# Performance work log

Measured on AMD Instinct MI355X. Metric: run time of the kernel, lower is better.

The kernel has to match this reference:

```python
import jax, jax.numpy as jnp
import numpy as np

LAM = 0.7      # lambda_param
GAM = 2.0      # gamma (weight upper bound)
ALPHA = 0.1    # age modulation scale
FGAM = 0.1     # fusion_gamma
SIGMAS = jnp.array([0.1, 0.5, 1.0, 2.0], dtype=jnp.float32)  # multi-kernel sigmas


def setup_inputs() -> dict:
    key = jax.random.key(0)
    ks = jax.random.split(key, 12)
    B, C, D, H, W, K = 12, 64, 32, 32, 32, 32
    mid, red = C // 2, C // 4
    Z = jax.random.normal(ks[0], (B, C, D, H, W), jnp.float32)
    masks = (jax.random.uniform(ks[1], (K, D, H, W)) > 0.5).astype(jnp.float32)
    masks = masks.at[:, 0, 0, 0].set(1.0)  # guarantee every region non-empty
    labels = jnp.arange(B, dtype=jnp.int32) % 3  # 4 samples each of CN/MCI/AD
    ages = 50.0 + 40.0 * jax.random.uniform(ks[2], (B,), jnp.float32)
    prior_weights = 1.0 + 0.1 * jax.random.normal(ks[3], (K,), jnp.float32)
    struct_w = 0.05 * jax.random.normal(ks[4], (mid, C), jnp.float32)
    noise_w = 0.05 * jax.random.normal(ks[5], (mid, C), jnp.float32)
    up_w = 0.05 * jax.random.normal(ks[6], (C, mid), jnp.float32)
    region_w = 0.05 * jax.random.normal(ks[7], (C, C, 3, 3, 3), jnp.float32)
    m_w1 = 0.05 * jax.random.normal(ks[8], (red, C), jnp.float32)
    m_b1 = jnp.zeros((red,), jnp.float32)
    m_w2 = 0.05 * jax.random.normal(ks[9], (C, red), jnp.float32)
    m_b2 = jnp.zeros((C,), jnp.float32)
    return dict(Z=Z, masks=masks, labels=labels, ages=ages, prior_weights=prior_weights,
                struct_w=struct_w, noise_w=noise_w, up_w=up_w, region_w=region_w,
                m_w1=m_w1, m_b1=m_b1, m_w2=m_w2, m_b2=m_b2)


def _mmd_pair(kern, ca, cb):
    # kern: [S,K,B,B] RBF kernels; ca/cb: [B] float class indicators.
    # Unbiased MMD^2 per region, averaged over sigmas -> [K].
    m = ca.sum()
    n = cb.sum()
    Kaa = jnp.einsum('skij,i,j->sk', kern, ca, ca)
    da = jnp.einsum('skii,i->sk', kern, ca)
    Kbb = jnp.einsum('skij,i,j->sk', kern, cb, cb)
    db = jnp.einsum('skii,i->sk', kern, cb)
    t1 = (Kaa - da) / (m * (m - 1.0))
    t2 = (Kbb - db) / (n * (n - 1.0))
    t3 = jnp.einsum('skij,i,j->sk', kern, ca, cb) * (-2.0 / (m * n))
    return (t1 + t2 + t3).mean(0)


def _forward(Z, masks, labels, ages, prior_weights, struct_w, noise_w, up_w,
             region_w, m_w1, m_b1, m_w2, m_b2):
    B, C = Z.shape[:2]
    K = masks.shape[0]
    # --- region-specific aggregation (fused segment-reduce over masks) ---
    msum = masks.sum((1, 2, 3))                                   # [K]
    rf = jnp.einsum('bcdhw,kdhw->bkc', Z, masks) / (msum[None, :, None] + 1e-6)
    # --- multi-class multi-kernel MMD per region ---
    x2 = jnp.sum(rf * rf, -1)                                     # [B,K]
    ip = jnp.einsum('ikc,jkc->kij', rf, rf)                       # [K,B,B]
    d2 = jnp.maximum(x2.T[:, :, None] + x2.T[:, None, :] - 2.0 * ip, 0.0)
    kern = jnp.exp(-d2[None] / (2.0 * SIGMAS[:, None, None, None] ** 2))  # [S,K,B,B]
    c_cn = (labels == 0).astype(jnp.float32)
    c_mci = (labels == 1).astype(jnp.float32)
    c_ad = (labels == 2).astype(jnp.float32)
    D_mmd = (_mmd_pair(kern, c_ad, c_cn) + _mmd_pair(kern, c_mci, c_cn)
             + _mmd_pair(kern, c_ad, c_mci))                      # [K]
    max_mmd = jnp.maximum(D_mmd.max(), 1e-6)
    nm = jnp.clip(D_mmd / max_mmd, 0.0)
    # symmetric KL between prior and MMD-evidence distributions (batchmean -> /K)
    lp = jax.nn.log_softmax(prior_weights)
    lq = jax.nn.log_softmax(nm)
    p = jnp.exp(lp)
    q = jnp.exp(lq)
    reg = 0.5 * jnp.sum(q * (lq - lp)) / K + 0.5 * jnp.sum(p * (lp - lq)) / K
    # --- prior-guided adaptive spatial weights ---
    base = LAM * prior_weights + (1.0 - LAM) * nm
    af = 1.0 + jax.nn.softplus(ALPHA * (ages - 50.0))             # [B]
    Wk = jax.nn.softmax(jnp.clip(base[None, :] * af[:, None], 0.0, GAM), axis=1)
    spatial = jnp.einsum('bk,kdhw->bdhw', Wk, masks)[:, None]     # [B,1,D,H,W]
    # --- orthogonal decomposition ---
    cs = jnp.einsum('oc,bcdhw->bodhw', struct_w, Z)               # 1x1x1 conv
    cnoise = jnp.einsum('oc,bcdhw->bodhw', noise_w, Z)
    s = cs.reshape(B, cs.shape[1], -1)
    n = cnoise.reshape(B, cnoise.shape[1], -1)
    eps = 1e-8
    cos = jnp.sum(s * n, -1) / (jnp.maximum(jnp.linalg.norm(s, axis=-1), eps)
                                * jnp.maximum(jnp.linalg.norm(n, axis=-1), eps))
    ortho = jnp.abs(cos).mean()
    Z_clean = jnp.einsum('oc,bcdhw->bodhw', up_w, cs)
    # --- region base field + 3x3x3 conv + channel modulation ---
    Zrb = jnp.einsum('bkc,kdhw->bcdhw', rf, masks)
    Zrec = jax.lax.conv_general_dilated(
        Zrb, region_w, (1, 1, 1), 'SAME',
        dimension_numbers=('NCDHW', 'OIDHW', 'NCDHW'))
    h = jax.nn.relu(jnp.einsum('bkc,rc->bkr', rf, m_w1) + m_b1)
    mod = jax.nn.softplus(jnp.einsum('bkr,cr->bkc', h, m_w2) + m_b2)  # [B,K,C]
    Zmod = Zrec * jnp.einsum('bkc,kdhw->bcdhw', mod, masks)
    Z_out = Z_clean + FGAM * (Zmod * spatial)
    return rf, spatial, Z_out, reg + ortho


def reference(Z, masks, labels, ages, prior_weights, struct_w, noise_w, up_w,
              region_w, m_w1, m_b1, m_w2, m_b2):
    return _forward(Z, masks, labels, ages, prior_weights, struct_w, noise_w,
                    up_w, region_w, m_w1, m_b1, m_w2, m_b2)
```

## Files before the change

kernel.cpp:

```cpp
#include <hip/hip_runtime.h>
#include <hip/hip_bf16.h>
#include <math.h>

#define REG_OFF    0
#define ORTHO_OFF  1
#define FLAG_OFF   2
#define MSUM_OFF   4
#define RF_OFF     64
#define G_OFF      24640
#define WKW_OFF    73792
#define MODTB_OFF  74176
#define M1TTH_OFF  86464
#define M1TTL_OFF  88512
#define WKCB_OFF   90560
#define IPK_OFF    422336
#define WS_TOTAL   426944
#define ZERO_FLOATS 73792

#define RF_OUT   0
#define SPAT_OUT 24576
#define ZOUT_OUT 417792
#define SCAL_OUT 25583616

typedef unsigned short u16;
typedef short bh8 __attribute__((ext_vector_type(8)));
typedef float fv4 __attribute__((ext_vector_type(4)));

__device__ __forceinline__ float bf2f(u16 u) {
  union { unsigned int i; float f; } x; x.i = ((unsigned int)u) << 16; return x.f;
}
__device__ __forceinline__ u16 f2bf(float f) {
  unsigned int u = __float_as_uint(f);
  return (u16)((u + 0x7fffu + ((u >> 16) & 1u)) >> 16);
}
__device__ __forceinline__ float ldin(const void* p, size_t i, bool f32) {
  return f32 ? ((const float*)p)[i] : bf2f(((const u16*)p)[i]);
}
__device__ __forceinline__ bh8 bits2bf8(unsigned int mbits) {
  union { bh8 v; unsigned int w[4]; } u;
#pragma unroll
  for (int j = 0; j < 4; j++) {
    unsigned int tt = mbits >> (2 * j);
    u.w[j] = ((tt & 1u) | ((tt & 2u) << 15)) * 0x3F80u;
  }
  return u.v;
}

__global__ void k_probe(const void* __restrict__ Z, float* __restrict__ ws) {
  int t = threadIdx.x;
  const u16* s = (const u16*)Z;
  float mx = 0.f;
  for (int i = t; i < 8192; i += 256) {
    float a = fabsf(bf2f(s[i]));
    if (!(a < 1e30f)) a = 3e38f;
    mx = fmaxf(mx, a);
  }
  __shared__ float r[256];
  r[t] = mx; __syncthreads();
  for (int o = 128; o > 0; o >>= 1) { if (t < o) r[t] = fmaxf(r[t], r[t + o]); __syncthreads(); }
  if (t == 0) ws[FLAG_OFF] = (r[0] > 1e6f) ? 1.f : 0.f;
}

__global__ void k_msum(const void* __restrict__ masks, float* __restrict__ ws) {
  int k = blockIdx.x, t = threadIdx.x;
  bool f32 = ws[FLAG_OFF] > 0.5f;
  float s = 0.f;
  for (int v = t; v < 32768; v += 256) s += ldin(masks, ((size_t)k << 15) + v, f32);
  __shared__ float red[256];
  red[t] = s; __syncthreads();
  for (int off = 128; off > 0; off >>= 1) { if (t < off) red[t] += red[t + off]; __syncthreads(); }
  if (t == 0) ws[MSUM_OFF + k] = red[0];
}

__global__ __launch_bounds__(256) void k_rfgram(const void* __restrict__ Z,
                                                const void* __restrict__ masks,
                                                float* __restrict__ ws) {
  __shared__ float Zt[64][68];
  __shared__ float Mt[64][36];
  int b = blockIdx.y, t = threadIdx.x;
  bool f32 = ws[FLAG_OFF] > 0.5f;
  int ci = t & 15, gj = t >> 4;
  int c0 = ci << 2, c20 = gj << 2, k0 = gj << 1;
  float accG[16], accR[8];
#pragma unroll
  for (int i = 0; i < 16; i++) accG[i] = 0.f;
#pragma unroll
  for (int i = 0; i < 8; i++) accR[i] = 0.f;
  int vs = blockIdx.x << 9;
  for (int t8 = 0; t8 < 8; t8++) {
    int vb = vs + (t8 << 6);
    __syncthreads();
    if (f32) {
      const float* Zf = (const float*)Z;
      const float* Mf = (const float*)masks;
#pragma unroll
      for (int i = 0; i < 8; i++) {
        int idx = (i << 8) + t, c = idx >> 5, v2 = (idx & 31) << 1;
        float2 u = *(const float2*)(Zf + (((size_t)(b << 6) + c) << 15) + vb + v2);
        Zt[v2][c] = u.x; Zt[v2 + 1][c] = u.y;
      }
#pragma unroll
      for (int i = 0; i < 4; i++) {
        int idx = (i << 8) + t, k = idx >> 5, v2 = (idx & 31) << 1;
        float2 u = *(const float2*)(Mf + ((size_t)k << 15) + vb + v2);
        Mt[v2][k] = u.x; Mt[v2 + 1][k] = u.y;
      }
    } else {
      const u16* Zs = (const u16*)Z;
      const u16* Ms = (const u16*)masks;
#pragma unroll
      for (int i = 0; i < 8; i++) {
        int idx = (i << 8) + t, c = idx >> 5, v2 = (idx & 31) << 1;
        unsigned int u = *(const unsigned int*)(Zs + (((size_t)(b << 6) + c) << 15) + vb + v2);
        Zt[v2][c]     = bf2f((u16)(u & 0xffff));
        Zt[v2 + 1][c] = bf2f((u16)(u >> 16));
      }
#pragma unroll
      for (int i = 0; i < 4; i++) {
        int idx = (i << 8) + t, k = idx >> 5, v2 = (idx & 31) << 1;
        unsigned int u = *(const unsigned int*)(Ms + ((size_t)k << 15) + vb + v2);
        Mt[v2][k]     = bf2f((u16)(u & 0xffff));
        Mt[v2 + 1][k] = bf2f((u16)(u >> 16));
      }
    }
    __syncthreads();
    for (int vt = 0; vt < 64; vt++) {
      float4 z1 = *(const float4*)&Zt[vt][c0];
      float4 z2 = *(const float4*)&Zt[vt][c20];
      float2 m2 = *(const float2*)&Mt[vt][k0];
      float z1a[4] = {z1.x, z1.y, z1.z, z1.w};
      float z2a[4] = {z2.x, z2.y, z2.z, z2.w};
      float m2a[2] = {m2.x, m2.y};
#pragma unroll
      for (int i = 0; i < 4; i++) {
#pragma unroll
        for (int j = 0; j < 4; j++) accG[(i << 2) + j] += z1a[i] * z2a[j];
#pragma unroll
        for (int kk = 0; kk < 2; kk++) accR[(i << 1) + kk] += z1a[i] * m2a[kk];
      }
    }
  }
  float* Gd = ws + G_OFF + (b << 12);
  float* Rd = ws + RF_OFF + (b << 11);
#pragma unroll
  for (int i = 0; i < 4; i++) {
#pragma unroll
    for (int j = 0; j < 4; j++) atomicAdd(Gd + ((c0 + i) << 6) + c20 + j, accG[(i << 2) + j]);
#pragma unroll
    for (int kk = 0; kk < 2; kk++) atomicAdd(Rd + ((k0 + kk) << 6) + c0 + i, accR[(i << 1) + kk]);
  }
}

__global__ void k_scale_rf(float* __restrict__ ws, float* __restrict__ out) {
  int i = blockIdx.x * 256 + threadIdx.x;
  int k = (i >> 6) & 31;
  float v = ws[RF_OFF + i] / (ws[MSUM_OFF + k] + 1e-6f);
  ws[RF_OFF + i] = v;
  out[RF_OUT + i] = v;
}

__global__ void k_ipk(float* __restrict__ ws) {
  __shared__ float rfk[12][65];
  int k = blockIdx.x, t = threadIdx.x;
  for (int i = t; i < 768; i += 256) {
    int b = i >> 6, c = i & 63;
    rfk[b][c] = ws[RF_OFF + (((size_t)(b << 5) + k) << 6) + c];
  }
  __syncthreads();
  if (t < 144) {
    int i = t / 12, j = t - (t / 12) * 12;
    float s = 0.f;
#pragma unroll
    for (int c = 0; c < 64; c++) s += rfk[i][c] * rfk[j][c];
    ws[IPK_OFF + k * 144 + t] = s;
  }
}

__global__ void k_mmdw(const int* __restrict__ labels, const void* __restrict__ ages,
                       const void* __restrict__ prior, float* __restrict__ ws) {
  __shared__ float IPL[32 * 145];
  __shared__ float dpart[128];
  __shared__ float Dm[32], nms[32], bases[32], pwl[32];
  __shared__ int labs[12];
  int t = threadIdx.x;
  bool f32 = ws[FLAG_OFF] > 0.5f;
  if (t < 12) labs[t] = labels[t];
  for (int i = t; i < 4608; i += 256) {
    int k = i / 144, r = i - k * 144;
    IPL[k * 145 + r] = ws[IPK_OFF + i];
  }
  __syncthreads();
  if (t < 128) {
    int k = t >> 2, s = t & 3;
    const float inv2s2[4] = {50.f, 2.f, 0.5f, 0.125f};
    float inv = inv2s2[s];
    const float* pk = IPL + k * 145;
    float c0 = 0.f, c1 = 0.f, c2 = 0.f;
#pragma unroll
    for (int i = 0; i < 12; i++) {
      int li = labs[i];
      c0 += (li == 0) ? 1.f : 0.f;
      c1 += (li == 1) ? 1.f : 0.f;
      c2 += (li == 2) ? 1.f : 0.f;
    }
    float s00=0,s01=0,s02=0,s10=0,s11=0,s12=0,s20=0,s21=0,s22=0;
    float dg0=0, dg1=0, dg2=0;
    for (int i = 0; i < 12; i++) {
      int li = labs[i];
      float x2i = pk[i * 13];
      float r0=0, r1=0, r2=0, dge=0;
      for (int j = 0; j < 12; j++) {
        float d2 = fmaxf(x2i + pk[j * 13] - 2.f * pk[i * 12 + j], 0.f);
        float e = expf(-d2 * inv);
        int lj = labs[j];
        r0 += (lj == 0) ? e : 0.f;
        r1 += (lj == 1) ? e : 0.f;
        r2 += (lj == 2) ? e : 0.f;
        if (j == i) dge = e;
      }
      if (li == 0)      { s00 += r0; s01 += r1; s02 += r2; dg0 += dge; }
      else if (li == 1) { s10 += r0; s11 += r1; s12 += r2; dg1 += dge; }
      else              { s20 += r0; s21 += r1; s22 += r2; dg2 += dge; }
    }
    float ta = (s22 - dg2) / (c2 * (c2 - 1.f));
    float tb = (s00 - dg0) / (c0 * (c0 - 1.f));
    float tc = (s11 - dg1) / (c1 * (c1 - 1.f));
    float dsum = (ta + tb - 2.f * s20 / (c2 * c0))
               + (tc + tb - 2.f * s10 / (c1 * c0))
               + (ta + tc - 2.f * s21 / (c2 * c1));
    dpart[t] = dsum;
  }
  __syncthreads();
  if (t < 32) {
    Dm[t] = (dpart[t * 4] + dpart[t * 4 + 1] + dpart[t * 4 + 2] + dpart[t * 4 + 3]) * 0.25f;
    pwl[t] = (float)ldin(prior, t, f32);
  }
  __syncthreads();
  if (t == 0) {
    float mx = 1e-6f;
    for (int k = 0; k < 32; k++) mx = fmaxf(mx, Dm[k]);
    float nmax = -1e30f, pmax = -1e30f;
    for (int k = 0; k < 32; k++) {
      nms[k] = fmaxf(Dm[k] / mx, 0.f);
      nmax = fmaxf(nmax, nms[k]);
      pmax = fmaxf(pmax, pwl[k]);
    }
    float nse = 0.f, pse = 0.f;
    for (int k = 0; k < 32; k++) { nse += expf(nms[k] - nmax); pse += expf(pwl[k] - pmax); }
    float lns = logf(nse), lps = logf(pse);
    float reg = 0.f;
    for (int k = 0; k < 32; k++) {
      float lqk = nms[k] - nmax - lns;
      float lpk = pwl[k] - pmax - lps;
      reg += 0.5f * (expf(lqk) * (lqk - lpk) + expf(lpk) * (lpk - lqk));
    }
    ws[REG_OFF] = reg / 32.f;
    for (int k = 0; k < 32; k++) bases[k] = 0.7f * pwl[k] + 0.3f * nms[k];
  }
  __syncthreads();
  if (t < 12) {
    float x = 0.1f * (ldin(ages, t, f32) - 50.f);
    float af = 1.f + fmaxf(x, 0.f) + log1pf(expf(-fabsf(x)));
    float w[32];
    float mx = -1e30f;
#pragma unroll
    for (int k = 0; k < 32; k++) {
      float v = fminf(fmaxf(bases[k] * af, 0.f), 2.f);
      w[k] = v; mx = fmaxf(mx, v);
    }
    float se = 0.f;
#pragma unroll
    for (int k = 0; k < 32; k++) se += expf(w[k] - mx);
#pragma unroll
    for (int k = 0; k < 32; k++) ws[WKW_OFF + (t << 5) + k] = expf(w[k] - mx) / se;
  }
}

__global__ __launch_bounds__(64) void k_mod(const void* __restrict__ m_w1, const void* __restrict__ m_b1,
                                            const void* __restrict__ m_w2, const void* __restrict__ m_b2,
                                            float* __restrict__ ws) {
  __shared__ float W1[16][65];
  __shared__ float W2T[16][64];
  __shared__ float B1[16], B2[64], RL[64], H[16];
  int bk = blockIdx.x, t = threadIdx.x;
  int bb = bk >> 5, kk = bk & 31;
  bool f32 = ws[FLAG_OFF] > 0.5f;
  for (int i = t; i < 1024; i += 64) {
    W1[i >> 6][i & 63] = ldin(m_w1, i, f32);
    W2T[i & 15][i >> 4] = ldin(m_w2, i, f32);
  }
  if (t < 16) B1[t] = ldin(m_b1, t, f32);
  B2[t] = ldin(m_b2, t, f32);
  RL[t] = ws[RF_OFF + (bk << 6) + t];
  __syncthreads();
  if (t < 16) {
    float s = B1[t];
#pragma unroll
    for (int c = 0; c < 64; c++) s += RL[c] * W1[t][c];
    H[t] = fmaxf(s, 0.f);
  }
  __syncthreads();
  {
    int c = t;
    float s = B2[c];
#pragma unroll
    for (int rr = 0; rr < 16; rr++) s += H[rr] * W2T[rr][c];
    float mv = fmaxf(s, 0.f) + log1pf(expf(-fabsf(s)));
    ((u16*)(ws + MODTB_OFF))[((size_t)bb * 64 + c) * 32 + kk] = f2bf(mv);
  }
}

__global__ void k_m1t(const void* __restrict__ struct_w, const void* __restrict__ up_w,
                      float* __restrict__ ws) {
  __shared__ float UPT[32][64];
  __shared__ float ST[32][64];
  int t = threadIdx.x, blk = blockIdx.x;
  bool f32 = ws[FLAG_OFF] > 0.5f;
  for (int i = t; i < 2048; i += 256) {
    UPT[i & 31][i >> 5] = ldin(up_w, i, f32);
    ST[i >> 6][i & 63] = ldin(struct_w, i, f32);
  }
  __syncthreads();
  int idx = (blk << 8) + t;
  int cin = idx >> 6, co = idx & 63;
  float s = 0.f;
#pragma unroll
  for (int j = 0; j < 32; j++) s += UPT[j][co] * ST[j][cin];
  u16 hi = f2bf(s);
  ((u16*)(ws + M1TTH_OFF))[co * 64 + cin] = hi;
  ((u16*)(ws + M1TTL_OFF))[co * 64 + cin] = f2bf(s - bf2f(hi));
}

__global__ void k_ortho(const void* __restrict__ sw, const void* __restrict__ nw,
                        float* __restrict__ ws) {
  int b = blockIdx.x >> 5, o = blockIdx.x & 31, c = threadIdx.x;
  bool f32 = ws[FLAG_OFF] > 0.5f;
  const float* Gb = ws + G_OFF + (b << 12);
  float ts = 0.f, tn = 0.f;
  for (int c2 = 0; c2 < 64; c2++) {
    float g = Gb[(c << 6) + c2];
    ts += g * ldin(sw, (o << 6) + c2, f32);
    tn += g * ldin(nw, (o << 6) + c2, f32);
  }
  float swc = ldin(sw, (o << 6) + c, f32);
  float nwc = ldin(nw, (o << 6) + c, f32);
  float ds = swc * tn, ss = swc * ts, nn = nwc * tn;
  for (int off = 32; off > 0; off >>= 1) {
    ds += __shfl_down(ds, off);
    ss += __shfl_down(ss, off);
    nn += __shfl_down(nn, off);
  }
  if (c == 0) {
    ss = fmaxf(ss, 0.f); nn = fmaxf(nn, 0.f);
    float cosv = ds / (fmaxf(sqrtf(ss), 1e-8f) * fmaxf(sqrtf(nn), 1e-8f));
    atomicAdd(ws + ORTHO_OFF, fabsf(cosv) * (1.f / 384.f));
  }
}

__global__ void k_wk(const void* __restrict__ rw, float* __restrict__ ws) {
  int bk = blockIdx.x;
  int b = bk >> 5, k = bk & 31;
  int t = threadIdx.x;
  bool f32 = ws[FLAG_OFF] > 0.5f;
  __shared__ float rl[64];
  if (t < 64) rl[t] = ws[RF_OFF + (bk << 6) + t];
  __syncthreads();
  u16* dst = (u16*)(ws + WKCB_OFF);
  for (int idx = t; idx < 1728; idx += 256) {
    int o = idx / 27, d = idx - o * 27;
    float s = 0.f;
    for (int c = 0; c < 64; c++) s += rl[c] * ldin(rw, (size_t)o * 1728 + c * 27 + d, f32);
    dst[(((size_t)b * 64 + o) * 27 + d) * 32 + k] = f2bf(s);
  }
}

__global__ void k_spatial(const void* __restrict__ masks, const float* __restrict__ ws,
                          float* __restrict__ out) {
  int b = blockIdx.y, t = threadIdx.x;
  bool f32 = ws[FLAG_OFF] > 0.5f;
  __shared__ float wl[32];
  if (t < 32) wl[t] = ws[WKW_OFF + (b << 5) + t];
  __syncthreads();
  int v0 = (blockIdx.x << 11) + (t << 3);
  float s[8] = {0, 0, 0, 0, 0, 0, 0, 0};
  for (int k = 0; k < 32; k++) {
    float wkv = wl[k];
    float mv[8];
    if (f32) {
      const float* Mf = (const float*)masks + ((size_t)k << 15) + v0;
      float4 a = *(const float4*)Mf, bb = *(const float4*)(Mf + 4);
      mv[0]=a.x; mv[1]=a.y; mv[2]=a.z; mv[3]=a.w; mv[4]=bb.x; mv[5]=bb.y; mv[6]=bb.z; mv[7]=bb.w;
    } else {
      uint4 u = *(const uint4*)((const u16*)masks + ((size_t)k << 15) + v0);
      mv[0]=bf2f((u16)(u.x & 0xffff)); mv[1]=bf2f((u16)(u.x >> 16));
      mv[2]=bf2f((u16)(u.y & 0xffff)); mv[3]=bf2f((u16)(u.y >> 16));
      mv[4]=bf2f((u16)(u.z & 0xffff)); mv[5]=bf2f((u16)(u.z >> 16));
      mv[6]=bf2f((u16)(u.w & 0xffff)); mv[7]=bf2f((u16)(u.w >> 16));
    }
#pragma unroll
    for (int j = 0; j < 8; j++) s[j] += wkv * mv[j];
  }
#pragma unroll
  for (int j = 0; j < 8; j++) out[SPAT_OUT + (b << 15) + v0 + j] = s[j];
}

__global__ __launch_bounds__(256, 4) void k_final(const void* __restrict__ Z,
                                                  const void* __restrict__ masks,
                                                  const float* __restrict__ ws,
                                                  float* __restrict__ out) {
  __shared__ unsigned int MHB[608];
  __shared__ float wl[32];
  __shared__ float spl[256];

  int b = blockIdx.y, tile = blockIdx.x, t = threadIdx.x;
  int lane = t & 63, w = t >> 6;
  int lo16 = lane & 15, g = lane >> 4, g8 = g << 3;
  bool f32 = ws[FLAG_OFF] > 0.5f;
  int d0 = (tile >> 4) << 2, h0 = ((tile >> 2) & 3) << 3, w0 = (tile & 3) << 3;

  for (int r = t; r < 600; r += 256) {
    int hd = r / 100, rr = r - hd * 100, hh = rr / 10, hw = rr - hh * 10;
    int gd = d0 - 1 + hd, gh = h0 - 1 + hh, gw = w0 - 1 + hw;
    unsigned int word = 0;
    if ((unsigned)gd < 32u && (unsigned)gh < 32u && (unsigned)gw < 32u) {
      size_t base = (size_t)(gd << 10) + (gh << 5) + gw;
#pragma unroll 4
      for (int k = 0; k < 32; k++) {
        float mv = ldin(masks, ((size_t)k << 15) + base, f32);
        word |= (mv != 0.f ? 1u : 0u) << k;
      }
    }
    MHB[r] = word;
  }
  if (t < 32) wl[t] = ws[WKW_OFF + (b << 5) + t];
  __syncthreads();

  {
    int dz = t >> 6, hy = (t >> 3) & 7, wx = t & 7;
    unsigned int m = MHB[dz * 100 + hy * 10 + wx + 111];
    float sp = 0.f;
#pragma unroll
    for (int k = 0; k < 32; k++) sp += ((m >> k) & 1u) ? wl[k] : 0.f;
    spl[t] = sp;
  }

  int hb4[4], v4[4];
#pragma unroll
  for (int pt = 0; pt < 4; pt++) {
    int pos = (w << 6) + (pt << 4) + lo16;
    int dz = pos >> 6, hy = (pos >> 3) & 7, wx = pos & 7;
    hb4[pt] = dz * 100 + hy * 10 + wx;
    v4[pt] = ((d0 + dz) << 10) + ((h0 + hy) << 5) + (w0 + wx);
  }

  fv4 acc[4][4];
#pragma unroll
  for (int ot = 0; ot < 4; ot++)
#pragma unroll
    for (int pt = 0; pt < 4; pt++) { acc[ot][pt][0]=0.f; acc[ot][pt][1]=0.f; acc[ot][pt][2]=0.f; acc[ot][pt][3]=0.f; }

  const u16* Wb = (const u16*)(ws + WKCB_OFF) + (size_t)b * 55296;
#pragma unroll 3
  for (int d = 0; d < 27; d++) {
    int da = d / 9, r9 = d - da * 9, db = r9 / 3, dc = r9 - db * 3;
    int off = da * 100 + db * 10 + dc;
    bh8 a[4];
#pragma unroll
    for (int ot = 0; ot < 4; ot++)
      a[ot] = *(const bh8*)(Wb + ((ot << 4) + lo16) * 864 + (d << 5) + g8);
#pragma unroll
    for (int pt = 0; pt < 4; pt++) {
      bh8 bv = bits2bf8(MHB[hb4[pt] + off] >> g8);
#pragma unroll
      for (int ot = 0; ot < 4; ot++)
        acc[ot][pt] = __builtin_amdgcn_mfma_f32_16x16x32_bf16(a[ot], bv, acc[ot][pt], 0, 0, 0);
    }
  }

  {
    const u16* modtb = (const u16*)(ws + MODTB_OFF);
    bh8 am[4];
#pragma unroll
    for (int ot = 0; ot < 4; ot++)
      am[ot] = *(const bh8*)(modtb + ((size_t)b * 64 + (ot << 4) + lo16) * 32 + g8);
    fv4 zero4; zero4[0]=0.f; zero4[1]=0.f; zero4[2]=0.f; zero4[3]=0.f;
#pragma unroll
    for (int pt = 0; pt < 4; pt++) {
      bh8 bc = bits2bf8(MHB[hb4[pt] + 111] >> g8);
      float spf = 0.1f * spl[(w << 6) + (pt << 4) + lo16];
#pragma unroll
      for (int ot = 0; ot < 4; ot++) {
        fv4 mm = __builtin_amdgcn_mfma_f32_16x16x32_bf16(am[ot], bc, zero4, 0, 0, 0);
        acc[ot][pt] = acc[ot][pt] * mm * spf;
      }
    }
  }

  {
    const u16* m1tth = (const u16*)(ws + M1TTH_OFF);
    const u16* m1ttl = (const u16*)(ws + M1TTL_OFF);
#pragma unroll 1
    for (int st = 0; st < 2; st++) {
      int cb = st << 5;
#pragma unroll
      for (int pt = 0; pt < 4; pt++) {
        bh8 bh, bl;
#pragma unroll
        for (int j = 0; j < 8; j++) {
          float zv = ldin(Z, (((size_t)(b << 6) + cb + g8 + j) << 15) + v4[pt], f32);
          u16 h = f2bf(zv);
          bh[j] = (short)h;
          bl[j] = (short)f2bf(zv - bf2f(h));
        }
#pragma unroll
        for (int ot = 0; ot < 4; ot++) {
          bh8 ah = *(const bh8*)(m1tth + ((ot << 4) + lo16) * 64 + cb + g8);
          bh8 al = *(const bh8*)(m1ttl + ((ot << 4) + lo16) * 64 + cb + g8);
          acc[ot][pt] = __builtin_amdgcn_mfma_f32_16x16x32_bf16(ah, bh, acc[ot][pt], 0, 0, 0);
          acc[ot][pt] = __builtin_amdgcn_mfma_f32_16x16x32_bf16(ah, bl, acc[ot][pt], 0, 0, 0);
          acc[ot][pt] = __builtin_amdgcn_mfma_f32_16x16x32_bf16(al, bh, acc[ot][pt], 0, 0, 0);
        }
      }
    }
  }

#pragma unroll
  for (int ot = 0; ot < 4; ot++)
#pragma unroll
    for (int pt = 0; pt < 4; pt++)
#pragma unroll
      for (int r = 0; r < 4; r++) {
        int o = (ot << 4) + (g << 2) + r;
        out[(size_t)ZOUT_OUT + (((size_t)(b << 6) + o) << 15) + v4[pt]] = acc[ot][pt][r];
      }
  if ((t | tile | b) == 0) out[SCAL_OUT] = ws[REG_OFF] + ws[ORTHO_OFF];
}

extern "C" void kernel_launch(void* const* d_in, const int* in_sizes, int n_in,
                              void* d_out, int out_size, void* d_ws, size_t ws_size,
                              hipStream_t stream) {
  (void)in_sizes; (void)n_in; (void)out_size; (void)ws_size;
  const void* Z        = d_in[0];
  const void* masks    = d_in[1];
  const int*  labels   = (const int*)d_in[2];
  const void* ages     = d_in[3];
  const void* prior    = d_in[4];
  const void* struct_w = d_in[5];
  const void* noise_w  = d_in[6];
  const void* up_w     = d_in[7];
  const void* region_w = d_in[8];
  const void* m_w1     = d_in[9];
  const void* m_b1     = d_in[10];
  const void* m_w2     = d_in[11];
  const void* m_b2     = d_in[12];
  float* ws = (float*)d_ws;
  float* out = (float*)d_out;

  hipMemsetAsync(d_ws, 0, (size_t)ZERO_FLOATS * 4, stream);
  k_probe<<<1, 256, 0, stream>>>(Z, ws);
  k_msum<<<32, 256, 0, stream>>>(masks, ws);
  k_rfgram<<<dim3(64, 12), 256, 0, stream>>>(Z, masks, ws);
  k_scale_rf<<<96, 256, 0, stream>>>(ws, out);
  k_m1t<<<16, 256, 0, stream>>>(struct_w, up_w, ws);
  k_ipk<<<32, 256, 0, stream>>>(ws);
  k_mmdw<<<1, 256, 0, stream>>>(labels, ages, prior, ws);
  k_mod<<<384, 64, 0, stream>>>(m_w1, m_b1, m_w2, m_b2, ws);
  k_ortho<<<384, 64, 0, stream>>>(struct_w, noise_w, ws);
  k_wk<<<384, 256, 0, stream>>>(region_w, ws);
  k_spatial<<<dim3(16, 12), 256, 0, stream>>>(masks, ws, out);
  k_final<<<dim3(128, 12), 256, 0, stream>>>(Z, masks, ws, out);
}
```

Measured before the change: 717.4 us.

## Precompute packed mask bitwords once and retile final conv by rows

Adds a kernel that packs the 32 region masks per voxel into one 32-bit word, stored in workspace. The final conv kernel then loads its halo from these words instead of reading 32 mask values per halo voxel in each of 1536 blocks. The tile shape also changes from 4x8x8 to 2x4x32, full-width rows, with a 4x6x40 halo, which lowers the halo overhead and makes row accesses contiguous. The cost is one extra small kernel launch and a 128KB workspace region.

```diff
diff --git a/kernel.cpp b/kernel.cpp
--- a/kernel.cpp
+++ b/kernel.cpp
@@ -14,7 +14,8 @@
 #define M1TTL_OFF  88512
 #define WKCB_OFF   90560
 #define IPK_OFF    422336
-#define WS_TOTAL   426944
+#define MB_OFF     426944
+#define WS_TOTAL   459712
 #define ZERO_FLOATS 73792
 
 #define RF_OUT   0
@@ -59,6 +60,18 @@
   r[t] = mx; __syncthreads();
   for (int o = 128; o > 0; o >>= 1) { if (t < o) r[t] = fmaxf(r[t], r[t + o]); __syncthreads(); }
   if (t == 0) ws[FLAG_OFF] = (r[0] > 1e6f) ? 1.f : 0.f;
+}
+
+__global__ void k_mb(const void* __restrict__ masks, float* __restrict__ ws) {
+  int v = blockIdx.x * 256 + threadIdx.x;
+  bool f32 = ws[FLAG_OFF] > 0.5f;
+  unsigned int word = 0;
+#pragma unroll 8
+  for (int k = 0; k < 32; k++) {
+    float mv = ldin(masks, ((size_t)k << 15) + v, f32);
+    word |= (mv != 0.f ? 1u : 0u) << k;
+  }
+  ((unsigned int*)(ws + MB_OFF))[v] = word;
 }
 
 __global__ void k_msum(const void* __restrict__ masks, float* __restrict__ ws) {
@@ -404,40 +417,37 @@
   for (int j = 0; j < 8; j++) out[SPAT_OUT + (b << 15) + v0 + j] = s[j];
 }
 
+#define MHW 40
 __global__ __launch_bounds__(256, 4) void k_final(const void* __restrict__ Z,
                                                   const void* __restrict__ masks,
                                                   const float* __restrict__ ws,
                                                   float* __restrict__ out) {
-  __shared__ unsigned int MHB[608];
+  __shared__ unsigned int MHB[4 * 6 * MHW];
   __shared__ float wl[32];
   __shared__ float spl[256];
+  (void)masks;
 
   int b = blockIdx.y, tile = blockIdx.x, t = threadIdx.x;
   int lane = t & 63, w = t >> 6;
   int lo16 = lane & 15, g = lane >> 4, g8 = g << 3;
-  bool f32 = ws[FLAG_OFF] > 0.5f;
-  int d0 = (tile >> 4) << 2, h0 = ((tile >> 2) & 3) << 3, w0 = (tile & 3) << 3;
-
-  for (int r = t; r < 600; r += 256) {
-    int hd = r / 100, rr = r - hd * 100, hh = rr / 10, hw = rr - hh * 10;
-    int gd = d0 - 1 + hd, gh = h0 - 1 + hh, gw = w0 - 1 + hw;
+  int d0 = (tile >> 3) << 1, h0 = (tile & 7) << 2;
+  const unsigned int* MB = (const unsigned int*)(ws + MB_OFF);
+  bool f32 = ws[FLAG_OFF] > 0.5f;
+
+  for (int i = t; i < 4 * 6 * MHW; i += 256) {
+    int hd = i / (6 * MHW), r = i - hd * (6 * MHW), hh = r / MHW, hw = r - hh * MHW;
+    int gd = d0 - 1 + hd, gh = h0 - 1 + hh, gw = hw - 1;
     unsigned int word = 0;
-    if ((unsigned)gd < 32u && (unsigned)gh < 32u && (unsigned)gw < 32u) {
-      size_t base = (size_t)(gd << 10) + (gh << 5) + gw;
-#pragma unroll 4
-      for (int k = 0; k < 32; k++) {
-        float mv = ldin(masks, ((size_t)k << 15) + base, f32);
-        word |= (mv != 0.f ? 1u : 0u) << k;
-      }
-    }
-    MHB[r] = word;
+    if ((unsigned)gd < 32u && (unsigned)gh < 32u && (unsigned)gw < 32u)
+      word = MB[(gd << 10) + (gh << 5) + gw];
+    MHB[i] = word;
   }
   if (t < 32) wl[t] = ws[WKW_OFF + (b << 5) + t];
   __syncthreads();
 
   {
-    int dz = t >> 6, hy = (t >> 3) & 7, wx = t & 7;
-    unsigned int m = MHB[dz * 100 + hy * 10 + wx + 111];
+    int dz = t >> 7, hy = (t >> 5) & 3, wx = t & 31;
+    unsigned int m = MHB[((dz + 1) * 6 + hy + 1) * MHW + wx + 1];
     float sp = 0.f;
 #pragma unroll
     for (int k = 0; k < 32; k++) sp += ((m >> k) & 1u) ? wl[k] : 0.f;
@@ -448,9 +458,9 @@
 #pragma unroll
   for (int pt = 0; pt < 4; pt++) {
     int pos = (w << 6) + (pt << 4) + lo16;
-    int dz = pos >> 6, hy = (pos >> 3) & 7, wx = pos & 7;
-    hb4[pt] = dz * 100 + hy * 10 + wx;
-    v4[pt] = ((d0 + dz) << 10) + ((h0 + hy) << 5) + (w0 + wx);
+    int dz = pos >> 7, hy = (pos >> 5) & 3, wx = pos & 31;
+    hb4[pt] = (dz * 6 + hy) * MHW + wx;
+    v4[pt] = ((d0 + dz) << 10) + ((h0 + hy) << 5) + wx;
   }
 
   fv4 acc[4][4];
@@ -463,7 +473,7 @@
 #pragma unroll 3
   for (int d = 0; d < 27; d++) {
     int da = d / 9, r9 = d - da * 9, db = r9 / 3, dc = r9 - db * 3;
-    int off = da * 100 + db * 10 + dc;
+    int off = (da * 6 + db) * MHW + dc;
     bh8 a[4];
 #pragma unroll
     for (int ot = 0; ot < 4; ot++)
@@ -486,7 +496,7 @@
     fv4 zero4; zero4[0]=0.f; zero4[1]=0.f; zero4[2]=0.f; zero4[3]=0.f;
 #pragma unroll
     for (int pt = 0; pt < 4; pt++) {
-      bh8 bc = bits2bf8(MHB[hb4[pt] + 111] >> g8);
+      bh8 bc = bits2bf8(MHB[hb4[pt] + 7 * MHW + 1] >> g8);
       float spf = 0.1f * spl[(w << 6) + (pt << 4) + lo16];
 #pragma unroll
       for (int ot = 0; ot < 4; ot++) {
@@ -558,6 +568,7 @@
 
   hipMemsetAsync(d_ws, 0, (size_t)ZERO_FLOATS * 4, stream);
   k_probe<<<1, 256, 0, stream>>>(Z, ws);
+  k_mb<<<128, 256, 0, stream>>>(masks, ws);
   k_msum<<<32, 256, 0, stream>>>(masks, ws);
   k_rfgram<<<dim3(64, 12), 256, 0, stream>>>(Z, masks, ws);
   k_scale_rf<<<96, 256, 0, stream>>>(ws, out);
```

Measured after the change: 619.7 us. 1.16x faster.
